# Kernel optimization log

Measured on AMD Instinct MI355X. Metric: run time of the kernel, lower is better.

Reference implementation:

```python
import jax, jax.numpy as jnp
import numpy as np

# dims
B, H, W = 2, 128, 256
MD = 34            # model_dim (last 2 channels = sin/cos lat)
LD = MD - 2        # learnable_dim = 32
NH, HD = 4, 8      # n_heads, head_dim
SH = 64            # shared_hidden (DISCO out channels)
K = 25             # number of DISCO basis functions (5x5 kernel_shape)
P = 7              # local stencil width (lat x lon support of geodesic basis)
R = P // 2
FF1, FF2 = 512, 256


def setup_inputs() -> dict:
    key = jax.random.key(0)
    ks = jax.random.split(key, 16)
    x = jax.random.normal(ks[0], (B, H, W, MD), dtype=jnp.float32)
    # latitude-dependent sparse geodesic basis values over a 7x7 stencil
    psi_val = jax.random.uniform(ks[1], (K, H, P * P), dtype=jnp.float32) * 0.1
    disco_w = jax.random.normal(ks[2], (SH, K), dtype=jnp.float32) * 0.1
    disco_b = jax.random.normal(ks[3], (SH,), dtype=jnp.float32) * 0.01
    # per-head MLP: shared_hidden -> 32 -> 1
    hw1 = jax.random.normal(ks[4], (NH, SH, 32), dtype=jnp.float32) * (1.0 / np.sqrt(SH))
    hb1 = jax.random.normal(ks[5], (NH, 32), dtype=jnp.float32) * 0.01
    hw2 = jax.random.normal(ks[6], (NH, 32, 1), dtype=jnp.float32) * (1.0 / np.sqrt(32))
    hb2 = jax.random.normal(ks[7], (NH, 1), dtype=jnp.float32) * 0.01
    # FFN: model_dim -> 512 -> 256 -> learnable_dim
    fw1 = jax.random.normal(ks[8], (MD, FF1), dtype=jnp.float32) * (1.0 / np.sqrt(MD))
    fw1 = fw1.at[-2:, :].set(0.0)  # matches ffn[0].weight[:, -2:] = 0 init
    fb1 = jax.random.normal(ks[9], (FF1,), dtype=jnp.float32) * 0.01
    fw2 = jax.random.normal(ks[10], (FF1, FF2), dtype=jnp.float32) * (1.0 / np.sqrt(FF1))
    fb2 = jax.random.normal(ks[11], (FF2,), dtype=jnp.float32) * 0.01
    fw3 = jax.random.normal(ks[12], (FF2, LD), dtype=jnp.float32) * (1.0 / np.sqrt(FF2))
    fb3 = jax.random.normal(ks[13], (LD,), dtype=jnp.float32) * 0.01
    return {"x": x, "psi_val": psi_val, "disco_w": disco_w, "disco_b": disco_b,
            "hw1": hw1, "hb1": hb1, "hw2": hw2, "hb2": hb2,
            "fw1": fw1, "fb1": fb1, "fw2": fw2, "fb2": fb2, "fw3": fw3, "fb3": fb3}


def _gelu(t):
    return jax.nn.gelu(t, approximate=False)  # torch nn.GELU default (erf)


def _disco_s2(xn, psi_val, disco_w, disco_b):
    """DISCO sparse-basis conv on single-channel maps.
    xn: (N, H, W). Basis values vary with output latitude, longitude is
    translation-invariant; support is a lat-clamped / lon-wrapped 7x7 stencil.
    Returns (N, SH, H, W)."""
    xp = jnp.pad(xn, ((0, 0), (R, R), (0, 0)), mode="edge")  # clamp at poles
    shifts = []
    for dlat in range(P):
        row = xp[:, dlat:dlat + H, :]
        for dlon in range(-R, R + 1):
            shifts.append(jnp.roll(row, -dlon, axis=2))  # wrap in longitude
    xs = jnp.stack(shifts, axis=1)  # (N, P*P, H, W)
    basis = jnp.einsum("khp,nphw->nkhw", psi_val, xs)       # basis aggregation
    return jnp.einsum("fk,nkhw->nfhw", disco_w, basis) + disco_b[None, :, None, None]


def reference(x, psi_val, disco_w, disco_b, hw1, hb1, hw2, hb2,
              fw1, fb1, fw2, fb2, fw3, fb3):
    x_learn = x[..., :LD]
    sin_cos = x[..., LD:]
    x_res = x_learn
    # (B,H,W,LD) -> (B*LD, H, W): each learnable channel is a 1-channel map
    xn = x_learn.transpose(0, 3, 1, 2).reshape(B * LD, H, W)
    d = _disco_s2(xn, psi_val, disco_w, disco_b)              # (B*LD, SH, H, W)
    d = d.reshape(B, LD, SH, H, W).transpose(0, 3, 4, 1, 2)    # (B,H,W,LD,SH)
    # per-head MLP over its head_dim slice (head index is outer in LD)
    d = d.reshape(B, H, W, NH, HD, SH)
    h = _gelu(jnp.einsum("bxynds,nso->bxyndo", d, hw1) + hb1[None, None, None, :, None, :])
    h = jnp.einsum("bxyndo,noe->bxynde", h, hw2) + hb2[None, None, None, :, None, :]
    x_learn = h[..., 0].reshape(B, H, W, LD)
    x_learn = x_learn + x_res                                  # use_residual
    x_full = jnp.concatenate([x_learn, sin_cos], axis=-1)
    x_res2 = x_learn
    t = _gelu(x_full @ fw1 + fb1)
    t = _gelu(t @ fw2 + fb2)
    t = t @ fw3 + fb3                                          # dropout p=0 -> id
    x_learn = t + x_res2
    return jnp.concatenate([x_learn, sin_cos], axis=-1)
```

## Files before the change

### kernel.cpp

```cpp
#include <hip/hip_runtime.h>
#include <math.h>


typedef __attribute__((ext_vector_type(8))) short bfrag;
typedef __attribute__((ext_vector_type(4))) float ffrag;
typedef __attribute__((ext_vector_type(4))) short short4v;

union bfi4 { int4 i; bfrag b; };

__device__ __forceinline__ float gelu_f(float v) {
  const float z = v * (2.3022077484f + 0.1029451564f * v * v);
  const float e = __builtin_amdgcn_exp2f(-z);
  return v * __builtin_amdgcn_rcpf(1.0f + e);
}

__device__ __forceinline__ short f2bf(float f) {
  union { float f; unsigned u; } v; v.f = f;
  unsigned r = (v.u + 0x7fffu + ((v.u >> 16) & 1u)) >> 16;
  return (short)r;
}

__device__ __forceinline__ short f2bf_fast(float f) {
  union { float f; unsigned u; } v; v.f = f;
  return (short)((v.u + 0x8000u) >> 16);
}

__device__ __forceinline__ float bf2f(short s) {
  union { float f; unsigned u; } v;
  v.u = ((unsigned)(unsigned short)s) << 16;
  return v.f;
}

__device__ __forceinline__ int pkbf(float a, float b) {
  union { float f; unsigned u; } va, vb; va.f = a; vb.f = b;
  return (int)__builtin_amdgcn_perm(vb.u + 0x8000u, va.u + 0x8000u, 0x07060302u);
}

template <int CTRL>
__device__ __forceinline__ float dpp_add(float v) {
  union { float f; int i; } s, t;
  s.f = v;
  t.i = __builtin_amdgcn_update_dpp(0, s.i, CTRL, 0xf, 0xf, true);
  return v + t.f;
}
__device__ __forceinline__ float reduce16(float v) {
  v = dpp_add<0xB1>(v);
  v = dpp_add<0x4E>(v);
  v = dpp_add<0x141>(v);
  v = dpp_add<0x140>(v);
  return v;
}

__device__ __forceinline__ void st4bf(short* p, float4 v) {
  short4v s;
  s[0] = f2bf(v.x); s[1] = f2bf(v.y); s[2] = f2bf(v.z); s[3] = f2bf(v.w);
  *(short4v*)p = s;
}

__global__ __launch_bounds__(256) void k01_prep(
    const float* __restrict__ psi, const float* __restrict__ dw,
    const float* __restrict__ db,
    const float* __restrict__ fw1, const float* __restrict__ fw2,
    const float* __restrict__ fw3, const float* __restrict__ hw1,
    const float* __restrict__ hb1,
    short* __restrict__ wcb, short* __restrict__ fw1s,
    short* __restrict__ fw2s, short* __restrict__ fw3s,
    short* __restrict__ hw1b, float* __restrict__ hb1e) {
  __shared__ __align__(16) char sm[33280];
  const int bid = blockIdx.x;
  const int tid = threadIdx.x;

  if (bid < 128) {
    float* psiL = (float*)sm;
    float* dwL  = (float*)(sm + 4928);
    const int h = bid;
    for (int e = tid; e < 1225; e += 256)
      psiL[e] = psi[(e / 49) * (128 * 49) + h * 49 + (e % 49)];
    for (int e = tid; e < 1600; e += 256) dwL[e] = dw[e];
    __syncthreads();
    short* outp = wcb + h * 8192;
    for (int idx = tid; idx < 8192; idx += 256) {
      const int jj = idx & 7, lane = (idx >> 3) & 63;
      const int nt = (idx >> 9) & 3, kt = (idx >> 11) & 1, par = idx >> 12;
      const int k = kt * 32 + (lane >> 4) * 8 + jj;
      const int f = nt * 16 + (lane & 15);
      const int r = k >> 3, dlt = k & 7;
      const int j = par ? (dlt - 1) : dlt;
      float acc = 0.f;
      if (r < 7 && j >= 0 && j < 7) {
        const int p = r * 7 + j;
#pragma unroll
        for (int kk = 0; kk < 25; ++kk)
          acc += dwL[f * 25 + kk] * psiL[kk * 49 + p];
      }
      outp[idx] = f2bf(acc);
    }
    return;
  }

  if (bid < 144) {
    short* S = (short*)sm;
    const int kt = bid - 128;
    const float* src = fw2 + kt * 8192;
    for (int q = tid; q < 2048; q += 256) {
      const int lin = q * 4;
      const int kk = lin >> 8, nn = lin & 255;
      st4bf(S + kk * 260 + nn, *(const float4*)(src + lin));
    }
    __syncthreads();
    short* dst = fw2s + kt * 8192;
    for (int q = tid; q < 8192; q += 256) {
      const int jj = q & 7, lane = (q >> 3) & 63, nt = q >> 9;
      const int kk = (lane >> 4) * 8 + jj, nn = nt * 16 + (lane & 15);
      dst[q] = S[kk * 260 + nn];
    }
    return;
  }

  if (bid == 144) {
    short* S = (short*)sm;
    for (int q = tid; q < 4096; q += 256) {
      const int lin = q * 4;
      const int kk = lin >> 9, nn = lin & 511;
      st4bf(S + kk * 516 + nn, *(const float4*)(fw1 + lin));
    }
    __syncthreads();
    for (int q = tid; q < 16384; q += 256) {
      const int jj = q & 7, lane = (q >> 3) & 63, nt = q >> 9;
      const int kk = (lane >> 4) * 8 + jj, nn = nt * 16 + (lane & 15);
      fw1s[q] = S[kk * 516 + nn];
    }
    return;
  }

  if (bid == 145) {
    short* S = (short*)sm;
    for (int q = tid; q < 2048; q += 256) {
      const int lin = q * 4;
      const int kk = lin >> 5, nn = lin & 31;
      st4bf(S + kk * 36 + nn, *(const float4*)(fw3 + lin));
    }
    __syncthreads();
    for (int q = tid; q < 8192; q += 256) {
      const int jj = q & 7, lane = (q >> 3) & 63;
      const int nt = (q >> 9) & 1, kt = q >> 10;
      const int kk = kt * 32 + (lane >> 4) * 8 + jj, nn = nt * 16 + (lane & 15);
      fw3s[q] = S[kk * 36 + nn];
    }
    return;
  }

  if (bid == 146) {
    short* S = (short*)sm;
    for (int q = tid; q < 2048; q += 256) {
      const int lin = q * 4;
      const int row = lin >> 5, nn = lin & 31;
      st4bf(S + row * 36 + nn, *(const float4*)(hw1 + lin));
    }
    __syncthreads();
    for (int q = tid; q < 8192; q += 256) {
      const int jj = q & 7, lane = (q >> 3) & 63;
      const int fr = (q >> 9) & 3, hd = q >> 11;
      const int kt = fr >> 1, nt = fr & 1;
      const int s = kt * 32 + (lane >> 4) * 8 + jj;
      const int forig = (s & 3) * 16 + (s >> 2);
      const int o = nt * 16 + (lane & 15);
      hw1b[q] = S[(hd * 64 + forig) * 36 + o];
    }
    return;
  }

  if (tid < 128) {
    const int n = tid >> 5, o = tid & 31;
    float acc = hb1[n * 32 + o];
#pragma unroll
    for (int s = 0; s < 64; ++s)
      acc += hw1[n * 2048 + s * 32 + o] * db[s];
    hb1e[tid] = acc;
  }
}

__global__ __launch_bounds__(256, 3) void k23_fused(
    const float* __restrict__ x,    const short* __restrict__ wcb,
    const short* __restrict__ hw1b, const float* __restrict__ hb1e,
    const float* __restrict__ hw2,  const float* __restrict__ hb2,
    const short* __restrict__ fw1s, const short* __restrict__ fw2s,
    const short* __restrict__ fw3s,
    const float* __restrict__ fb1,  const float* __restrict__ fb2,
    const float* __restrict__ fb3,  float* __restrict__ outb) {
  __shared__ __align__(16) char smem[52352];
  short* sX  = (short*)smem;
  short* sM  = (short*)(smem + 50176);

  const int tid = threadIdx.x;
  const int w0  = blockIdx.x * 32;
  const int h   = blockIdx.y;
  const int b   = blockIdx.z;

  {
    int4* p = (int4*)sX;
    int4 z; z.x = z.y = z.z = z.w = 0;
    for (int e = tid; e < (32 * 388) / 8; e += 256) p[e] = z;
  }
  __syncthreads();

#pragma unroll 1
  for (int r = 0; r < 7; ++r) {
    int hr = h - 3 + r; hr = hr < 0 ? 0 : (hr > 127 ? 127 : hr);
    const float* __restrict__ xrow = x + (size_t)((b * 128 + hr) * 256) * 34;
    short* __restrict__ sxr = sX + r * 48;
    for (int e = tid; e < 39 * 16; e += 256) {
      const int c2 = e & 15;
      const int wp = e >> 4;
      const int wr = (w0 - 3 + wp) & 255;
      const float2 v = *(const float2*)&xrow[wr * 34 + c2 * 2];
      short* dp = sxr + (c2 * 2) * 388 + wp;
      dp[0]   = f2bf_fast(v.x);
      dp[388] = f2bf_fast(v.y);
    }
  }

  if (tid < 64) {
    const int wl = tid >> 1;
    const int sc = tid & 1;
    const int idx = ((b * 128 + h) * 256 + (w0 + wl)) * 34 + 32 + sc;
    outb[idx] = x[idx];
  }
  __syncthreads();

  const int lane = tid & 63, lm = lane & 15, lq = lane >> 4;
  const int n = tid >> 6;
  const int rowbase = ((b * 128 + h) * 256) * 34;

  float hb1v[2], hw2v[2];
#pragma unroll
  for (int nt = 0; nt < 2; ++nt) {
    hb1v[nt] = hb1e[n * 32 + nt * 16 + lm];
    hw2v[nt] = hw2[n * 32 + nt * 16 + lm];
  }
  const float hb2n = hb2[n];

  bfrag cB[2][2][4];
#pragma unroll
  for (int par = 0; par < 2; ++par)
#pragma unroll
    for (int kt = 0; kt < 2; ++kt)
#pragma unroll
      for (int nt = 0; nt < 4; ++nt)
        cB[par][kt][nt] = *(const bfrag*)(wcb + h * 8192 +
                            ((par * 2 + kt) * 4 + nt) * 512 + lane * 8);
  bfrag mB[2][2];
#pragma unroll
  for (int kt = 0; kt < 2; ++kt)
#pragma unroll
    for (int nt = 0; nt < 2; ++nt)
      mB[kt][nt] = *(const bfrag*)(hw1b + n * 2048 + (kt * 2 + nt) * 512 + lane * 8);

  short* sDw = (short*)(smem + 24832) + n * (2 * 1152);
  const int* tpB = (const int*)sX;

  auto ldtaps = [&](int c, bfi4& u0, bfi4& u1) {
    const int base0 = c * 194 + lq * 24 + lm;
    u0.i.x = tpB[base0];      u0.i.y = tpB[base0 + 1];
    u0.i.z = tpB[base0 + 2];  u0.i.w = tpB[base0 + 3];
    u1.i.x = tpB[base0 + 96]; u1.i.y = tpB[base0 + 97];
    u1.i.z = tpB[base0 + 98]; u1.i.w = tpB[base0 + 99];
  };
  auto convf = [&](const bfi4& u0, const bfi4& u1, int par, ffrag* d) {
#pragma unroll
    for (int nt = 0; nt < 4; ++nt) d[nt] = ffrag{0.f, 0.f, 0.f, 0.f};
#pragma unroll
    for (int nt = 0; nt < 4; ++nt) {
      d[nt] = __builtin_amdgcn_mfma_f32_16x16x32_bf16(u0.b, cB[par][0][nt], d[nt], 0, 0, 0);
      d[nt] = __builtin_amdgcn_mfma_f32_16x16x32_bf16(u1.b, cB[par][1][nt], d[nt], 0, 0, 0);
    }
  };
  auto writeD = [&](const ffrag* d, short* buf) {
#pragma unroll
    for (int rr = 0; rr < 4; ++rr) {
      int2 w;
      w.x = pkbf(d[0][rr], d[1][rr]);
      w.y = pkbf(d[2][rr], d[3][rr]);
      *(int2*)(buf + (lq * 4 + rr) * 72 + lm * 4) = w;
    }
  };
  auto mlpStage = [&](const short* buf, int i, int par) {
    bfrag a10 = *(const bfrag*)(buf + lm * 72 + lq * 8);
    bfrag a11 = *(const bfrag*)(buf + lm * 72 + 32 + lq * 8);
    ffrag h10 = {0.f, 0.f, 0.f, 0.f}, h11 = {0.f, 0.f, 0.f, 0.f};
    h10 = __builtin_amdgcn_mfma_f32_16x16x32_bf16(a10, mB[0][0], h10, 0, 0, 0);
    h10 = __builtin_amdgcn_mfma_f32_16x16x32_bf16(a11, mB[1][0], h10, 0, 0, 0);
    h11 = __builtin_amdgcn_mfma_f32_16x16x32_bf16(a10, mB[0][1], h11, 0, 0, 0);
    h11 = __builtin_amdgcn_mfma_f32_16x16x32_bf16(a11, mB[1][1], h11, 0, 0, 0);
    const int c = n * 8 + i;
#pragma unroll
    for (int rr = 0; rr < 4; ++rr) {
      float v = gelu_f(h10[rr] + hb1v[0]) * hw2v[0] +
                gelu_f(h11[rr] + hb1v[1]) * hw2v[1];
      v = reduce16(v);
      if (lm == 0) {
        const int p = 2 * (lq * 4 + rr) + par;
        const float res = x[rowbase + (w0 + p) * 34 + c];
        sM[p * 34 + c] = f2bf_fast(v + hb2n + res);
      }
    }
  };

  bfi4 u0, u1;
  ldtaps(n * 8, u0, u1);
  ffrag dA[4], dB[4];
  convf(u0, u1, 0, dA);
#pragma unroll 1
  for (int i = 0; i < 8; ++i) {
    short* b0 = sDw;
    short* b1 = sDw + 1152;
    writeD(dA, b0);
    convf(u0, u1, 1, dB);
    mlpStage(b0, i, 0);
    writeD(dB, b1);
    if (i < 7) {
      ldtaps(n * 8 + i + 1, u0, u1);
      convf(u0, u1, 0, dA);
    }
    mlpStage(b1, i, 1);
  }
  __syncthreads();

  short* sT1 = (short*)smem;
  short* sT2 = (short*)(smem + 33280);
  const int wave = n;
  const int koff = lq * 8;
  const int mt3 = wave & 1;
  const int nt3 = wave >> 1;
  const int col3 = nt3 * 16 + lm;
  const int pixg = (b * 128 + h) * 256 + w0;

  bfrag aF[2];
#pragma unroll
  for (int mt = 0; mt < 2; ++mt)
    aF[mt] = *(const bfrag*)(sM + (mt * 16 + lm) * 34 + koff);
  bfrag b1f[8];
#pragma unroll
  for (int ni = 0; ni < 8; ++ni)
    b1f[ni] = *(const bfrag*)(fw1s + (wave * 8 + ni) * 512 + lane * 8);
  bfrag w3f[8];
#pragma unroll
  for (int kt = 0; kt < 8; ++kt)
    w3f[kt] = *(const bfrag*)(fw3s + nt3 * 512 + kt * 1024 + lane * 8);
  float res3[4];
#pragma unroll
  for (int r = 0; r < 4; ++r)
    res3[r] = bf2f(sM[(mt3 * 16 + lq * 4 + r) * 34 + col3]);

#pragma unroll
  for (int ni = 0; ni < 8; ++ni) {
    const int nt = wave * 8 + ni;
#pragma unroll
    for (int mt = 0; mt < 2; ++mt) {
      ffrag c = {0.f, 0.f, 0.f, 0.f};
      c = __builtin_amdgcn_mfma_f32_16x16x32_bf16(aF[mt], b1f[ni], c, 0, 0, 0);
      const int col = nt * 16 + lm;
      const float bias = fb1[col];
#pragma unroll
      for (int r = 0; r < 4; ++r) {
        const int row = mt * 16 + lq * 4 + r;
        sT1[row * 520 + col] = f2bf_fast(gelu_f(c[r] + bias));
      }
    }
  }
  __syncthreads();

  const int n0 = wave * 4;
  ffrag acc[2][4];
#pragma unroll
  for (int mt = 0; mt < 2; ++mt)
#pragma unroll
    for (int ni = 0; ni < 4; ++ni) acc[mt][ni] = ffrag{0.f, 0.f, 0.f, 0.f};

  const short* sA0 = &sT1[lm * 520 + koff];
  const short* sA1 = sA0 + 16 * 520;
  const short* w2p = fw2s + n0 * 512 + lane * 8;

  bfrag bv[4];
#pragma unroll
  for (int ni = 0; ni < 4; ++ni)
    bv[ni] = *(const bfrag*)(w2p + ni * 512);

#pragma unroll 2
  for (int kt = 0; kt < 16; ++kt) {
    bfrag bnext[4];
    if (kt < 15) {
#pragma unroll
      for (int ni = 0; ni < 4; ++ni)
        bnext[ni] = *(const bfrag*)(w2p + (kt + 1) * 8192 + ni * 512);
    }
    const bfrag a0 = *(const bfrag*)(sA0 + kt * 32);
    const bfrag a1 = *(const bfrag*)(sA1 + kt * 32);
#pragma unroll
    for (int ni = 0; ni < 4; ++ni) {
      acc[0][ni] = __builtin_amdgcn_mfma_f32_16x16x32_bf16(a0, bv[ni], acc[0][ni], 0, 0, 0);
      acc[1][ni] = __builtin_amdgcn_mfma_f32_16x16x32_bf16(a1, bv[ni], acc[1][ni], 0, 0, 0);
    }
    if (kt < 15) {
#pragma unroll
      for (int ni = 0; ni < 4; ++ni) bv[ni] = bnext[ni];
    }
  }
#pragma unroll
  for (int mt = 0; mt < 2; ++mt)
#pragma unroll
    for (int ni = 0; ni < 4; ++ni) {
      const int col = (n0 + ni) * 16 + lm;
      const float bias = fb2[col];
#pragma unroll
      for (int r = 0; r < 4; ++r) {
        const int row = mt * 16 + lq * 4 + r;
        sT2[row * 264 + col] = f2bf_fast(gelu_f(acc[mt][ni][r] + bias));
      }
    }
  __syncthreads();

  ffrag c3 = {0.f, 0.f, 0.f, 0.f};
  const short* sA3 = &sT2[(mt3 * 16 + lm) * 264 + koff];
#pragma unroll
  for (int kt = 0; kt < 8; ++kt) {
    const bfrag a = *(const bfrag*)(sA3 + kt * 32);
    c3 = __builtin_amdgcn_mfma_f32_16x16x32_bf16(a, w3f[kt], c3, 0, 0, 0);
  }
  {
    const float bias = fb3[col3];
#pragma unroll
    for (int r = 0; r < 4; ++r) {
      const int row = mt3 * 16 + lq * 4 + r;
      outb[(pixg + row) * 34 + col3] = c3[r] + bias + res3[r];
    }
  }
}

extern "C" void kernel_launch(void* const* d_in, const int* in_sizes, int n_in,
                              void* d_out, int out_size, void* d_ws, size_t ws_size,
                              hipStream_t stream) {
  const float* x   = (const float*)d_in[0];
  const float* psi = (const float*)d_in[1];
  const float* dw  = (const float*)d_in[2];
  const float* db  = (const float*)d_in[3];
  const float* hw1 = (const float*)d_in[4];
  const float* hb1 = (const float*)d_in[5];
  const float* hw2 = (const float*)d_in[6];
  const float* hb2 = (const float*)d_in[7];
  const float* fw1 = (const float*)d_in[8];
  const float* fb1 = (const float*)d_in[9];
  const float* fw2 = (const float*)d_in[10];
  const float* fb2 = (const float*)d_in[11];
  const float* fw3 = (const float*)d_in[12];
  const float* fb3 = (const float*)d_in[13];
  float* outb = (float*)d_out;

  short* wcb  = (short*)d_ws;
  short* fw1s = wcb + 1048576;
  short* fw2s = fw1s + 16384;
  short* fw3s = fw2s + 131072;
  short* hw1b = fw3s + 8192;
  float* hb1e = (float*)(hw1b + 8192);

  hipLaunchKernelGGL(k01_prep, dim3(148), dim3(256), 0, stream,
                     psi, dw, db, fw1, fw2, fw3, hw1, hb1,
                     wcb, fw1s, fw2s, fw3s, hw1b, hb1e);
  hipLaunchKernelGGL(k23_fused, dim3(8, 128, 2), dim3(256), 0, stream,
                     x, wcb, hw1b, hb1e, hw2, hb2,
                     fw1s, fw2s, fw3s, fb1, fb2, fb3, outb);
}
```

Before: 199.0 us.

## Shrink shared memory and registers in fused kernel to raise occupancy

Raises the launch bound in the fused kernel from 3 to 4 blocks per CU and cuts shared memory from about 52KB to 36KB. To fit, FFN layer 1 is computed in two 256-column halves interleaved with layer 2, and the conv/MLP software pipeline is dropped in favour of a simple sequential loop over a single buffer. The residual is read from the bf16 staged tile instead of global memory, and fw1/fw3 fragments are loaded on demand instead of held in registers. The prep kernel now computes the per-latitude combined weights once into a tile rather than recomputing them for every output slot. In exchange the kernel loses its conv/MLP overlap, adds extra barriers and takes the residual from bf16 data, which changes precision slightly.

```diff
diff --git a/kernel.cpp b/kernel.cpp
--- a/kernel.cpp
+++ b/kernel.cpp
@@ -71,29 +71,35 @@
   const int tid = threadIdx.x;
 
   if (bid < 128) {
-    float* psiL = (float*)sm;
-    float* dwL  = (float*)(sm + 4928);
+    short* tile = (short*)sm;
     const int h = bid;
-    for (int e = tid; e < 1225; e += 256)
-      psiL[e] = psi[(e / 49) * (128 * 49) + h * 49 + (e % 49)];
-    for (int e = tid; e < 1600; e += 256) dwL[e] = dw[e];
+    const int lane = tid & 63;
+    const int w = __builtin_amdgcn_readfirstlane(tid >> 6);
+    float dwreg[25];
+#pragma unroll
+    for (int kk = 0; kk < 25; ++kk) dwreg[kk] = dw[lane * 25 + kk];
+    const int p0 = w * 13;
+    const int pend = (p0 + 13 < 49) ? (p0 + 13) : 49;
+#pragma unroll 1
+    for (int p = p0; p < pend; ++p) {
+      float acc = 0.f;
+#pragma unroll
+      for (int kk = 0; kk < 25; ++kk)
+        acc += dwreg[kk] * psi[kk * 6272 + h * 49 + p];
+      tile[lane * 52 + p] = f2bf(acc);
+    }
     __syncthreads();
     short* outp = wcb + h * 8192;
     for (int idx = tid; idx < 8192; idx += 256) {
-      const int jj = idx & 7, lane = (idx >> 3) & 63;
+      const int jj = idx & 7, ln = (idx >> 3) & 63;
       const int nt = (idx >> 9) & 3, kt = (idx >> 11) & 1, par = idx >> 12;
-      const int k = kt * 32 + (lane >> 4) * 8 + jj;
-      const int f = nt * 16 + (lane & 15);
+      const int k = kt * 32 + (ln >> 4) * 8 + jj;
+      const int f = nt * 16 + (ln & 15);
       const int r = k >> 3, dlt = k & 7;
       const int j = par ? (dlt - 1) : dlt;
-      float acc = 0.f;
-      if (r < 7 && j >= 0 && j < 7) {
-        const int p = r * 7 + j;
-#pragma unroll
-        for (int kk = 0; kk < 25; ++kk)
-          acc += dwL[f * 25 + kk] * psiL[kk * 49 + p];
-      }
-      outp[idx] = f2bf(acc);
+      short v = 0;
+      if (r < 7 && j >= 0 && j < 7) v = tile[f * 52 + r * 7 + j];
+      outp[idx] = v;
     }
     return;
   }
@@ -180,7 +186,7 @@
   }
 }
 
-__global__ __launch_bounds__(256, 3) void k23_fused(
+__global__ __launch_bounds__(256, 4) void k23_fused(
     const float* __restrict__ x,    const short* __restrict__ wcb,
     const short* __restrict__ hw1b, const float* __restrict__ hb1e,
     const float* __restrict__ hw2,  const float* __restrict__ hb2,
@@ -188,9 +194,9 @@
     const short* __restrict__ fw3s,
     const float* __restrict__ fb1,  const float* __restrict__ fb2,
     const float* __restrict__ fb3,  float* __restrict__ outb) {
-  __shared__ __align__(16) char smem[52352];
-  short* sX  = (short*)smem;
-  short* sM  = (short*)(smem + 50176);
+  __shared__ __align__(16) char smem[36224];
+  short* sX = (short*)smem;
+  short* sM = (short*)(smem + 34048);
 
   const int tid = threadIdx.x;
   const int w0  = blockIdx.x * 32;
@@ -230,7 +236,6 @@
 
   const int lane = tid & 63, lm = lane & 15, lq = lane >> 4;
   const int n = tid >> 6;
-  const int rowbase = ((b * 128 + h) * 256) * 34;
 
   float hb1v[2], hw2v[2];
 #pragma unroll
@@ -256,78 +261,62 @@
     for (int nt = 0; nt < 2; ++nt)
       mB[kt][nt] = *(const bfrag*)(hw1b + n * 2048 + (kt * 2 + nt) * 512 + lane * 8);
 
-  short* sDw = (short*)(smem + 24832) + n * (2 * 1152);
+  short* sDw = (short*)(smem + 24832) + n * 1152;
   const int* tpB = (const int*)sX;
 
-  auto ldtaps = [&](int c, bfi4& u0, bfi4& u1) {
+#pragma unroll 1
+  for (int i = 0; i < 8; ++i) {
+    const int c = n * 8 + i;
+
     const int base0 = c * 194 + lq * 24 + lm;
+    bfi4 u0, u1;
     u0.i.x = tpB[base0];      u0.i.y = tpB[base0 + 1];
     u0.i.z = tpB[base0 + 2];  u0.i.w = tpB[base0 + 3];
     u1.i.x = tpB[base0 + 96]; u1.i.y = tpB[base0 + 97];
     u1.i.z = tpB[base0 + 98]; u1.i.w = tpB[base0 + 99];
-  };
-  auto convf = [&](const bfi4& u0, const bfi4& u1, int par, ffrag* d) {
-#pragma unroll
-    for (int nt = 0; nt < 4; ++nt) d[nt] = ffrag{0.f, 0.f, 0.f, 0.f};
-#pragma unroll
-    for (int nt = 0; nt < 4; ++nt) {
-      d[nt] = __builtin_amdgcn_mfma_f32_16x16x32_bf16(u0.b, cB[par][0][nt], d[nt], 0, 0, 0);
-      d[nt] = __builtin_amdgcn_mfma_f32_16x16x32_bf16(u1.b, cB[par][1][nt], d[nt], 0, 0, 0);
-    }
-  };
-  auto writeD = [&](const ffrag* d, short* buf) {
-#pragma unroll
-    for (int rr = 0; rr < 4; ++rr) {
-      int2 w;
-      w.x = pkbf(d[0][rr], d[1][rr]);
-      w.y = pkbf(d[2][rr], d[3][rr]);
-      *(int2*)(buf + (lq * 4 + rr) * 72 + lm * 4) = w;
-    }
-  };
-  auto mlpStage = [&](const short* buf, int i, int par) {
-    bfrag a10 = *(const bfrag*)(buf + lm * 72 + lq * 8);
-    bfrag a11 = *(const bfrag*)(buf + lm * 72 + 32 + lq * 8);
-    ffrag h10 = {0.f, 0.f, 0.f, 0.f}, h11 = {0.f, 0.f, 0.f, 0.f};
-    h10 = __builtin_amdgcn_mfma_f32_16x16x32_bf16(a10, mB[0][0], h10, 0, 0, 0);
-    h10 = __builtin_amdgcn_mfma_f32_16x16x32_bf16(a11, mB[1][0], h10, 0, 0, 0);
-    h11 = __builtin_amdgcn_mfma_f32_16x16x32_bf16(a10, mB[0][1], h11, 0, 0, 0);
-    h11 = __builtin_amdgcn_mfma_f32_16x16x32_bf16(a11, mB[1][1], h11, 0, 0, 0);
-    const int c = n * 8 + i;
-#pragma unroll
-    for (int rr = 0; rr < 4; ++rr) {
-      float v = gelu_f(h10[rr] + hb1v[0]) * hw2v[0] +
-                gelu_f(h11[rr] + hb1v[1]) * hw2v[1];
-      v = reduce16(v);
-      if (lm == 0) {
+
+#pragma unroll
+    for (int par = 0; par < 2; ++par) {
+      ffrag dacc[4];
+#pragma unroll
+      for (int nt = 0; nt < 4; ++nt) dacc[nt] = ffrag{0.f, 0.f, 0.f, 0.f};
+#pragma unroll
+      for (int nt = 0; nt < 4; ++nt) {
+        dacc[nt] = __builtin_amdgcn_mfma_f32_16x16x32_bf16(u0.b, cB[par][0][nt], dacc[nt], 0, 0, 0);
+        dacc[nt] = __builtin_amdgcn_mfma_f32_16x16x32_bf16(u1.b, cB[par][1][nt], dacc[nt], 0, 0, 0);
+      }
+
+#pragma unroll
+      for (int rr = 0; rr < 4; ++rr) {
+        int2 w;
+        w.x = pkbf(dacc[0][rr], dacc[1][rr]);
+        w.y = pkbf(dacc[2][rr], dacc[3][rr]);
+        *(int2*)(sDw + (lq * 4 + rr) * 72 + lm * 4) = w;
+      }
+
+      bfrag a10 = *(const bfrag*)(sDw + lm * 72 + lq * 8);
+      bfrag a11 = *(const bfrag*)(sDw + lm * 72 + 32 + lq * 8);
+      ffrag h10 = {0.f, 0.f, 0.f, 0.f}, h11 = {0.f, 0.f, 0.f, 0.f};
+      h10 = __builtin_amdgcn_mfma_f32_16x16x32_bf16(a10, mB[0][0], h10, 0, 0, 0);
+      h10 = __builtin_amdgcn_mfma_f32_16x16x32_bf16(a11, mB[1][0], h10, 0, 0, 0);
+      h11 = __builtin_amdgcn_mfma_f32_16x16x32_bf16(a10, mB[0][1], h11, 0, 0, 0);
+      h11 = __builtin_amdgcn_mfma_f32_16x16x32_bf16(a11, mB[1][1], h11, 0, 0, 0);
+
+#pragma unroll
+      for (int rr = 0; rr < 4; ++rr) {
+        float v = gelu_f(h10[rr] + hb1v[0]) * hw2v[0] +
+                  gelu_f(h11[rr] + hb1v[1]) * hw2v[1];
+        v = reduce16(v);
         const int p = 2 * (lq * 4 + rr) + par;
-        const float res = x[rowbase + (w0 + p) * 34 + c];
-        sM[p * 34 + c] = f2bf_fast(v + hb2n + res);
-      }
-    }
-  };
-
-  bfi4 u0, u1;
-  ldtaps(n * 8, u0, u1);
-  ffrag dA[4], dB[4];
-  convf(u0, u1, 0, dA);
-#pragma unroll 1
-  for (int i = 0; i < 8; ++i) {
-    short* b0 = sDw;
-    short* b1 = sDw + 1152;
-    writeD(dA, b0);
-    convf(u0, u1, 1, dB);
-    mlpStage(b0, i, 0);
-    writeD(dB, b1);
-    if (i < 7) {
-      ldtaps(n * 8 + i + 1, u0, u1);
-      convf(u0, u1, 0, dA);
-    }
-    mlpStage(b1, i, 1);
+        const float res = bf2f(sX[c * 388 + 144 + 3 + p]);
+        if (lm == 0) sM[p * 34 + c] = f2bf_fast(v + hb2n + res);
+      }
+    }
   }
   __syncthreads();
 
-  short* sT1 = (short*)smem;
-  short* sT2 = (short*)(smem + 33280);
+  short* sT1h = (short*)smem;
+  short* sT2  = (short*)(smem + 16896);
   const int wave = n;
   const int koff = lq * 8;
   const int mt3 = wave & 1;
@@ -339,73 +328,60 @@
 #pragma unroll
   for (int mt = 0; mt < 2; ++mt)
     aF[mt] = *(const bfrag*)(sM + (mt * 16 + lm) * 34 + koff);
-  bfrag b1f[8];
-#pragma unroll
-  for (int ni = 0; ni < 8; ++ni)
-    b1f[ni] = *(const bfrag*)(fw1s + (wave * 8 + ni) * 512 + lane * 8);
-  bfrag w3f[8];
-#pragma unroll
-  for (int kt = 0; kt < 8; ++kt)
-    w3f[kt] = *(const bfrag*)(fw3s + nt3 * 512 + kt * 1024 + lane * 8);
   float res3[4];
 #pragma unroll
   for (int r = 0; r < 4; ++r)
     res3[r] = bf2f(sM[(mt3 * 16 + lq * 4 + r) * 34 + col3]);
 
-#pragma unroll
-  for (int ni = 0; ni < 8; ++ni) {
-    const int nt = wave * 8 + ni;
-#pragma unroll
-    for (int mt = 0; mt < 2; ++mt) {
-      ffrag c = {0.f, 0.f, 0.f, 0.f};
-      c = __builtin_amdgcn_mfma_f32_16x16x32_bf16(aF[mt], b1f[ni], c, 0, 0, 0);
-      const int col = nt * 16 + lm;
-      const float bias = fb1[col];
-#pragma unroll
-      for (int r = 0; r < 4; ++r) {
-        const int row = mt * 16 + lq * 4 + r;
-        sT1[row * 520 + col] = f2bf_fast(gelu_f(c[r] + bias));
-      }
-    }
-  }
-  __syncthreads();
-
   const int n0 = wave * 4;
   ffrag acc[2][4];
 #pragma unroll
   for (int mt = 0; mt < 2; ++mt)
 #pragma unroll
     for (int ni = 0; ni < 4; ++ni) acc[mt][ni] = ffrag{0.f, 0.f, 0.f, 0.f};
-
-  const short* sA0 = &sT1[lm * 520 + koff];
-  const short* sA1 = sA0 + 16 * 520;
-  const short* w2p = fw2s + n0 * 512 + lane * 8;
-
-  bfrag bv[4];
-#pragma unroll
-  for (int ni = 0; ni < 4; ++ni)
-    bv[ni] = *(const bfrag*)(w2p + ni * 512);
+  const short* w2base = fw2s + n0 * 512 + lane * 8;
+
+#pragma unroll 1
+  for (int H = 0; H < 2; ++H) {
+    bfrag b1f[4];
+#pragma unroll
+    for (int ni = 0; ni < 4; ++ni)
+      b1f[ni] = *(const bfrag*)(fw1s + (H * 16 + wave * 4 + ni) * 512 + lane * 8);
+#pragma unroll
+    for (int ni = 0; ni < 4; ++ni) {
+      const int ntl = wave * 4 + ni;
+#pragma unroll
+      for (int mt = 0; mt < 2; ++mt) {
+        ffrag cc = {0.f, 0.f, 0.f, 0.f};
+        cc = __builtin_amdgcn_mfma_f32_16x16x32_bf16(aF[mt], b1f[ni], cc, 0, 0, 0);
+        const int colg = H * 256 + ntl * 16 + lm;
+        const float bias = fb1[colg];
+#pragma unroll
+        for (int r = 0; r < 4; ++r) {
+          const int row = mt * 16 + lq * 4 + r;
+          sT1h[row * 264 + ntl * 16 + lm] = f2bf_fast(gelu_f(cc[r] + bias));
+        }
+      }
+    }
+    __syncthreads();
 
 #pragma unroll 2
-  for (int kt = 0; kt < 16; ++kt) {
-    bfrag bnext[4];
-    if (kt < 15) {
+    for (int kt = 0; kt < 8; ++kt) {
+      bfrag bv[4];
 #pragma unroll
       for (int ni = 0; ni < 4; ++ni)
-        bnext[ni] = *(const bfrag*)(w2p + (kt + 1) * 8192 + ni * 512);
-    }
-    const bfrag a0 = *(const bfrag*)(sA0 + kt * 32);
-    const bfrag a1 = *(const bfrag*)(sA1 + kt * 32);
-#pragma unroll
-    for (int ni = 0; ni < 4; ++ni) {
-      acc[0][ni] = __builtin_amdgcn_mfma_f32_16x16x32_bf16(a0, bv[ni], acc[0][ni], 0, 0, 0);
-      acc[1][ni] = __builtin_amdgcn_mfma_f32_16x16x32_bf16(a1, bv[ni], acc[1][ni], 0, 0, 0);
-    }
-    if (kt < 15) {
-#pragma unroll
-      for (int ni = 0; ni < 4; ++ni) bv[ni] = bnext[ni];
-    }
-  }
+        bv[ni] = *(const bfrag*)(w2base + (H * 8 + kt) * 8192 + ni * 512);
+      const bfrag a0 = *(const bfrag*)(sT1h + lm * 264 + kt * 32 + koff);
+      const bfrag a1 = *(const bfrag*)(sT1h + (16 + lm) * 264 + kt * 32 + koff);
+#pragma unroll
+      for (int ni = 0; ni < 4; ++ni) {
+        acc[0][ni] = __builtin_amdgcn_mfma_f32_16x16x32_bf16(a0, bv[ni], acc[0][ni], 0, 0, 0);
+        acc[1][ni] = __builtin_amdgcn_mfma_f32_16x16x32_bf16(a1, bv[ni], acc[1][ni], 0, 0, 0);
+      }
+    }
+    __syncthreads();
+  }
+
 #pragma unroll
   for (int mt = 0; mt < 2; ++mt)
 #pragma unroll
@@ -421,11 +397,12 @@
   __syncthreads();
 
   ffrag c3 = {0.f, 0.f, 0.f, 0.f};
-  const short* sA3 = &sT2[(mt3 * 16 + lm) * 264 + koff];
+  const short* sA3 = sT2 + (mt3 * 16 + lm) * 264 + koff;
 #pragma unroll
   for (int kt = 0; kt < 8; ++kt) {
     const bfrag a = *(const bfrag*)(sA3 + kt * 32);
-    c3 = __builtin_amdgcn_mfma_f32_16x16x32_bf16(a, w3f[kt], c3, 0, 0, 0);
+    const bfrag bw = *(const bfrag*)(fw3s + nt3 * 512 + kt * 1024 + lane * 8);
+    c3 = __builtin_amdgcn_mfma_f32_16x16x32_bf16(a, bw, c3, 0, 0, 0);
   }
   {
     const float bias = fb3[col3];
```

Result: faster. 170.3 us (-14.4%).
